# Performance work log

Measured on AMD Instinct MI355X. Metric: run time of the kernel, lower is better.

## Reference

```python
import jax, jax.numpy as jnp
import numpy as np

DT = 0.01
THETA = 1.0 / (2.0 - 2.0 ** (1.0 / 3.0))
C1 = THETA / 2.0
C2 = (1.0 - THETA) / 2.0
C3 = (1.0 - THETA) / 2.0
C4 = THETA / 2.0
D1 = THETA
D2 = 1.0 - 2.0 * THETA
D3 = THETA

B, DIM, RANK = 4096, 1024, 256


def setup_inputs() -> dict:
    key = jax.random.key(0)
    k0, k1, k2, k3, k4 = jax.random.split(key, 5)
    x = jax.random.normal(k0, (B, DIM), jnp.float32)
    v = jax.random.normal(k1, (B, DIM), jnp.float32)
    force = jax.random.normal(k2, (B, DIM), jnp.float32)
    # small-scale low-rank Christoffel factors for numerical stability over steps
    U = jax.random.normal(k3, (DIM, RANK), jnp.float32) * 0.02
    W = jax.random.normal(k4, (RANK, DIM), jnp.float32) * 0.02
    return {"x": x, "v": v, "force": force, "U": U, "W": W, "steps": 4}


def reference(x, v, force, U, W, steps):
    dt = DT  # dt_scale = 1.0

    def christoffel(tv, tx):
        # low-rank quadratic form in velocity: Gamma(v)_k = sum_r W[r,k] * ((v @ U)_r)^2
        h = tv @ U              # [B, RANK]
        return (h * h) @ W      # [B, DIM]

    def acceleration(tx, tv):
        return -christoffel(tv, tx) + force

    curr_x, curr_v = x, v
    for _ in range(steps):  # steps is a small static Python int
        x1 = curr_x + C1 * dt * curr_v
        v1 = curr_v + D1 * dt * acceleration(x1, curr_v)
        x2 = x1 + C2 * dt * v1
        v2 = v1 + D2 * dt * acceleration(x2, v1)
        x3 = x2 + C3 * dt * v2
        v3 = v2 + D3 * dt * acceleration(x3, v2)
        curr_x = x3 + C4 * dt * v3
        curr_v = v3
    return (curr_x, curr_v)
```

## Files before the change

kernel.cpp:

```cpp
#include <hip/hip_runtime.h>

typedef unsigned short ushort_t;
typedef float f32x4 __attribute__((ext_vector_type(4)));
typedef short s16x8 __attribute__((ext_vector_type(8)));

#define BROWS 4096
#define DIMK  1024
#define RANKK 256
#define TROWS 16
#define GPAD  (RANKK + 8)

#define DTF 0.01f
#define THETAF 1.35120719195965763f
#define C1F    0.675603595979828816f
#define C2F   (-0.175603595979828816f)
#define D1F    1.35120719195965763f
#define D2F   (-1.70241438391931526f)

__device__ __forceinline__ ushort_t f2bf(float f) {
    unsigned u = __builtin_bit_cast(unsigned, f);
    return (ushort_t)((u + 0x7FFFu + ((u >> 16) & 1u)) >> 16);
}

__global__ void fr_transpose_cast(const float* __restrict__ in,
                                  ushort_t* __restrict__ out, int R, int C) {
    __shared__ float tile[32][33];
    int tiles_c = C >> 5;
    int tr = blockIdx.x / tiles_c;
    int tc = blockIdx.x % tiles_c;
    int tx = threadIdx.x & 31;
    int ty = threadIdx.x >> 5;
#pragma unroll
    for (int i = 0; i < 32; i += 8)
        tile[ty + i][tx] = in[(size_t)(tr * 32 + ty + i) * C + tc * 32 + tx];
    __syncthreads();
#pragma unroll
    for (int i = 0; i < 32; i += 8)
        out[(size_t)(tc * 32 + ty + i) * R + tr * 32 + tx] = f2bf(tile[tx][ty + i]);
}

__global__ __launch_bounds__(512, 2) void fr_kernel(
    const float* __restrict__ x_in, const float* __restrict__ v_in,
    const float* __restrict__ f_in, const ushort_t* __restrict__ Ut,
    const ushort_t* __restrict__ Wt, const int* __restrict__ steps_p,
    float* __restrict__ out) {
    __shared__ ushort_t vb[TROWS * DIMK];
    __shared__ ushort_t gb[TROWS * GPAD];

    const int tid  = threadIdx.x;
    const int lane = tid & 63;
    const int wave = tid >> 6;
    const int m16  = lane & 15;
    const int g4   = lane >> 4;
    const int row0 = blockIdx.x * TROWS;
    const int n_acc = 3 * steps_p[0];

    float vreg[32], xreg[32], freg[32];
#pragma unroll
    for (int nt = 0; nt < 8; ++nt) {
#pragma unroll
        for (int r = 0; r < 4; ++r) {
            const int m = g4 * 4 + r;
            const int n = wave * 128 + nt * 16 + m16;
            const size_t gi = (size_t)(row0 + m) * DIMK + n;
            const float v0 = v_in[gi];
            vreg[nt * 4 + r] = v0;
            xreg[nt * 4 + r] = x_in[gi] + (C1F * DTF) * v0;
            freg[nt * 4 + r] = f_in[gi];
            vb[m * DIMK + (n ^ ((m & 7) << 3))] = f2bf(v0);
        }
    }
    __syncthreads();

    const s16x8* b0p = (const s16x8*)(Ut + (size_t)(wave * 32 + m16) * DIMK + g4 * 8);
    const s16x8* b1p = b0p + (16 * DIMK) / 8;
    const s16x8* bwp = (const s16x8*)(Wt + (size_t)(wave * 128 + m16) * RANKK + g4 * 8);
    const int n1a = wave * 32 + m16;
    const int n1b = n1a + 16;

    for (int j = 0; j < n_acc; ++j) {
        f32x4 h0 = {0.f, 0.f, 0.f, 0.f}, h1 = {0.f, 0.f, 0.f, 0.f};
#pragma unroll 8
        for (int kk = 0; kk < DIMK / 32; ++kk) {
            const int k0 = kk * 32 + g4 * 8;
            const s16x8 a = *(const s16x8*)&vb[m16 * DIMK + (k0 ^ ((m16 & 7) << 3))];
            const s16x8 b0 = b0p[kk * 4];
            const s16x8 b1 = b1p[kk * 4];
            h0 = __builtin_amdgcn_mfma_f32_16x16x32_bf16(a, b0, h0, 0, 0, 0);
            h1 = __builtin_amdgcn_mfma_f32_16x16x32_bf16(a, b1, h1, 0, 0, 0);
        }
#pragma unroll
        for (int r = 0; r < 4; ++r) {
            const int m = g4 * 4 + r;
            gb[m * GPAD + n1a] = f2bf(h0[r] * h0[r]);
            gb[m * GPAD + n1b] = f2bf(h1[r] * h1[r]);
        }
        __syncthreads();

        f32x4 acc[8];
#pragma unroll
        for (int nt = 0; nt < 8; ++nt) acc[nt] = (f32x4){0.f, 0.f, 0.f, 0.f};
#pragma unroll 2
        for (int kk = 0; kk < RANKK / 32; ++kk) {
            const int k0 = kk * 32 + g4 * 8;
            const s16x8 a = *(const s16x8*)&gb[m16 * GPAD + k0];
#pragma unroll
            for (int nt = 0; nt < 8; ++nt) {
                const s16x8 b = bwp[nt * 512 + kk * 4];
                acc[nt] = __builtin_amdgcn_mfma_f32_16x16x32_bf16(a, b, acc[nt], 0, 0, 0);
            }
        }

        const int ph = j - (j / 3) * 3;
        const float ddt = ((ph == 0) ? D1F : (ph == 1) ? D2F : D1F) * DTF;
        const float cdt = ((ph == 2) ? ((j == n_acc - 1) ? C1F : THETAF) : C2F) * DTF;
#pragma unroll
        for (int nt = 0; nt < 8; ++nt) {
#pragma unroll
            for (int r = 0; r < 4; ++r) {
                const int i = nt * 4 + r;
                const int m = g4 * 4 + r;
                const int n = wave * 128 + nt * 16 + m16;
                const float vn = vreg[i] + ddt * (freg[i] - acc[nt][r]);
                vreg[i] = vn;
                xreg[i] += cdt * vn;
                vb[m * DIMK + (n ^ ((m & 7) << 3))] = f2bf(vn);
            }
        }
        __syncthreads();
    }

    float* xo = out;
    float* vo = out + (size_t)BROWS * DIMK;
#pragma unroll
    for (int nt = 0; nt < 8; ++nt) {
#pragma unroll
        for (int r = 0; r < 4; ++r) {
            const int i = nt * 4 + r;
            const int m = g4 * 4 + r;
            const int n = wave * 128 + nt * 16 + m16;
            const size_t gi = (size_t)(row0 + m) * DIMK + n;
            xo[gi] = xreg[i];
            vo[gi] = vreg[i];
        }
    }
}

extern "C" void kernel_launch(void* const* d_in, const int* in_sizes, int n_in,
                              void* d_out, int out_size, void* d_ws, size_t ws_size,
                              hipStream_t stream) {
    const float* x = (const float*)d_in[0];
    const float* v = (const float*)d_in[1];
    const float* f = (const float*)d_in[2];
    const float* U = (const float*)d_in[3];
    const float* W = (const float*)d_in[4];
    const int* steps = (const int*)d_in[5];

    ushort_t* Ut = (ushort_t*)d_ws;
    ushort_t* Wt = Ut + (size_t)RANKK * DIMK;
    float* out = (float*)d_out;

    fr_transpose_cast<<<(DIMK / 32) * (RANKK / 32), 256, 0, stream>>>(U, Ut, DIMK, RANKK);
    fr_transpose_cast<<<(RANKK / 32) * (DIMK / 32), 256, 0, stream>>>(W, Wt, RANKK, DIMK);
    fr_kernel<<<BROWS / TROWS, 512, 0, stream>>>(x, v, f, Ut, Wt, steps, out);
}
```

Baseline: 369.3 us.

## Use 1024-thread blocks with software-pipelined weight prefetch and LDS-staged state

Doubles the block to 16 waves, so each wave owns 64 output columns and 16 rank columns. U and W are pre-packed into an MFMA-fragment-contiguous bf16 layout, and their fragments are prefetched in a rotating four-buffer register pipeline that runs across the two GEMM phases and iterations. x and force move out of registers into LDS (force packed as bf16) to cut register pressure. MFMAs are issued through inline asm with AGPR accumulators, and barriers become a raw lgkmcnt wait plus s_barrier. The cost is an LDS footprint of about 130KB, which limits occupancy to one block per CU, and the force term now loses precision from bf16 rounding.

```diff
diff --git a/kernel.cpp b/kernel.cpp
--- a/kernel.cpp
+++ b/kernel.cpp
@@ -1,6 +1,7 @@
 #include <hip/hip_runtime.h>
 
 typedef unsigned short ushort_t;
+typedef unsigned int u32;
 typedef float f32x4 __attribute__((ext_vector_type(4)));
 typedef short s16x8 __attribute__((ext_vector_type(8)));
 
@@ -8,7 +9,6 @@
 #define DIMK  1024
 #define RANKK 256
 #define TROWS 16
-#define GPAD  (RANKK + 8)
 
 #define DTF 0.01f
 #define THETAF 1.35120719195965763f
@@ -21,126 +21,182 @@
     unsigned u = __builtin_bit_cast(unsigned, f);
     return (ushort_t)((u + 0x7FFFu + ((u >> 16) & 1u)) >> 16);
 }
-
-__global__ void fr_transpose_cast(const float* __restrict__ in,
-                                  ushort_t* __restrict__ out, int R, int C) {
-    __shared__ float tile[32][33];
-    int tiles_c = C >> 5;
-    int tr = blockIdx.x / tiles_c;
-    int tc = blockIdx.x % tiles_c;
-    int tx = threadIdx.x & 31;
-    int ty = threadIdx.x >> 5;
-#pragma unroll
-    for (int i = 0; i < 32; i += 8)
-        tile[ty + i][tx] = in[(size_t)(tr * 32 + ty + i) * C + tc * 32 + tx];
-    __syncthreads();
-#pragma unroll
-    for (int i = 0; i < 32; i += 8)
-        out[(size_t)(tc * 32 + ty + i) * R + tr * 32 + tx] = f2bf(tile[tx][ty + i]);
-}
-
-__global__ __launch_bounds__(512, 2) void fr_kernel(
+__device__ __forceinline__ u32 pack2bf(float lo, float hi) {
+    return (u32)f2bf(lo) | ((u32)f2bf(hi) << 16);
+}
+__device__ __forceinline__ float unpk_lo(u32 u) {
+    return __builtin_bit_cast(float, u << 16);
+}
+__device__ __forceinline__ float unpk_hi(u32 u) {
+    return __builtin_bit_cast(float, u & 0xFFFF0000u);
+}
+
+__device__ __forceinline__ f32x4 mfma_agpr(s16x8 a, s16x8 b, f32x4 c) {
+    asm("v_mfma_f32_16x16x32_bf16 %0, %1, %2, %0" : "+a"(c) : "v"(a), "v"(b));
+    return c;
+}
+
+#define BAR() asm volatile("s_waitcnt lgkmcnt(0)\n\ts_barrier" ::: "memory")
+
+__global__ void fr_pack_u(const float* __restrict__ U, ushort_t* __restrict__ Ut2) {
+    const int o = blockIdx.x * 256 + threadIdx.x;
+    const int e = o & 7, g4 = (o >> 3) & 3, kk = (o >> 5) & 31;
+    const int m16 = (o >> 10) & 15, w = (o >> 14) & 15;
+    const int n = w * 16 + m16, k = kk * 32 + g4 * 8 + e;
+    Ut2[o] = f2bf(U[k * RANKK + n]);
+}
+__global__ void fr_pack_w(const float* __restrict__ W, ushort_t* __restrict__ Wt2) {
+    const int o = blockIdx.x * 256 + threadIdx.x;
+    const int e = o & 7, g4 = (o >> 3) & 3, nt = (o >> 5) & 3;
+    const int s = (o >> 7) & 7, m16 = (o >> 10) & 15, w = (o >> 14) & 15;
+    const int n = w * 64 + nt * 16 + m16, k = s * 32 + g4 * 8 + e;
+    Wt2[o] = f2bf(W[k * DIMK + n]);
+}
+
+
+#define L1(t, BUF) do {                                                       \
+    BUF[0] = *(const s16x8*)(up + (2 * (t)) * 32);                            \
+    BUF[1] = *(const s16x8*)(up + (2 * (t) + 1) * 32);                        \
+} while (0)
+
+#define G1(t, BUF) do {                                                       \
+    { const s16x8 a_ = *(const s16x8*)&vb[m16 * DIMK + (((2*(t))*32 + g4*8) ^ swz)];   \
+      h0 = mfma_agpr(a_, BUF[0], h0); }                                       \
+    { const s16x8 a_ = *(const s16x8*)&vb[m16 * DIMK + (((2*(t)+1)*32 + g4*8) ^ swz)]; \
+      h0 = mfma_agpr(a_, BUF[1], h0); }                                       \
+} while (0)
+
+#define L2(u, BUF) do {                                                       \
+    BUF[0] = *(const s16x8*)(wp + ((u) >> 1) * 128 + (((u) & 1) * 2) * 32);   \
+    BUF[1] = *(const s16x8*)(wp + ((u) >> 1) * 128 + (((u) & 1) * 2 + 1) * 32);\
+} while (0)
+
+#define G2(u, A2, BUF) do {                                                   \
+    acc[((u) & 1) * 2]     = mfma_agpr(A2, BUF[0], acc[((u) & 1) * 2]);       \
+    acc[((u) & 1) * 2 + 1] = mfma_agpr(A2, BUF[1], acc[((u) & 1) * 2 + 1]);   \
+} while (0)
+
+#define ARD(s) (*(const s16x8*)&gb[m16 * RANKK + (((s) * 32 + g4 * 8) ^ swz)])
+
+__global__ __launch_bounds__(1024) void fr_kernel(
     const float* __restrict__ x_in, const float* __restrict__ v_in,
-    const float* __restrict__ f_in, const ushort_t* __restrict__ Ut,
-    const ushort_t* __restrict__ Wt, const int* __restrict__ steps_p,
+    const float* __restrict__ f_in, const ushort_t* __restrict__ Ut2,
+    const ushort_t* __restrict__ Wt2, const int* __restrict__ steps_p,
     float* __restrict__ out) {
     __shared__ ushort_t vb[TROWS * DIMK];
-    __shared__ ushort_t gb[TROWS * GPAD];
+    __shared__ ushort_t gb[TROWS * RANKK];
+    __shared__ float    xs[TROWS * DIMK];
+    __shared__ u32      fb[8 * 1024];
 
     const int tid  = threadIdx.x;
     const int lane = tid & 63;
     const int wave = tid >> 6;
     const int m16  = lane & 15;
     const int g4   = lane >> 4;
+    const int swz  = (m16 & 7) << 3;
     const int row0 = blockIdx.x * TROWS;
     const int n_acc = 3 * steps_p[0];
 
-    float vreg[32], xreg[32], freg[32];
-#pragma unroll
-    for (int nt = 0; nt < 8; ++nt) {
+    float vreg[16], xdelta[16];
+#pragma unroll
+    for (int nt = 0; nt < 4; ++nt) {
+        float fv[4];
 #pragma unroll
         for (int r = 0; r < 4; ++r) {
             const int m = g4 * 4 + r;
-            const int n = wave * 128 + nt * 16 + m16;
+            const int n = wave * 64 + nt * 16 + m16;
             const size_t gi = (size_t)(row0 + m) * DIMK + n;
             const float v0 = v_in[gi];
-            vreg[nt * 4 + r] = v0;
-            xreg[nt * 4 + r] = x_in[gi] + (C1F * DTF) * v0;
-            freg[nt * 4 + r] = f_in[gi];
+            vreg[nt * 4 + r]   = v0;
+            xdelta[nt * 4 + r] = (C1F * DTF) * v0;
+            xs[m * DIMK + n]   = x_in[gi];
+            fv[r] = f_in[gi];
             vb[m * DIMK + (n ^ ((m & 7) << 3))] = f2bf(v0);
         }
+        fb[(nt * 2 + 0) * 1024 + tid] = pack2bf(fv[0], fv[1]);
+        fb[(nt * 2 + 1) * 1024 + tid] = pack2bf(fv[2], fv[3]);
     }
+
+    const ushort_t* up = Ut2 + (wave * 16 + m16) * 1024 + g4 * 8;
+    const ushort_t* wp = Wt2 + (wave * 16 + m16) * 1024 + g4 * 8;
+
+    s16x8 bA[2], bB[2], bC[2], bD[2];
+    L1(0, bA); L1(1, bB); L1(2, bC); L1(3, bD);
     __syncthreads();
 
-    const s16x8* b0p = (const s16x8*)(Ut + (size_t)(wave * 32 + m16) * DIMK + g4 * 8);
-    const s16x8* b1p = b0p + (16 * DIMK) / 8;
-    const s16x8* bwp = (const s16x8*)(Wt + (size_t)(wave * 128 + m16) * RANKK + g4 * 8);
-    const int n1a = wave * 32 + m16;
-    const int n1b = n1a + 16;
-
+    f32x4 acc[4];
     for (int j = 0; j < n_acc; ++j) {
-        f32x4 h0 = {0.f, 0.f, 0.f, 0.f}, h1 = {0.f, 0.f, 0.f, 0.f};
-#pragma unroll 8
-        for (int kk = 0; kk < DIMK / 32; ++kk) {
-            const int k0 = kk * 32 + g4 * 8;
-            const s16x8 a = *(const s16x8*)&vb[m16 * DIMK + (k0 ^ ((m16 & 7) << 3))];
-            const s16x8 b0 = b0p[kk * 4];
-            const s16x8 b1 = b1p[kk * 4];
-            h0 = __builtin_amdgcn_mfma_f32_16x16x32_bf16(a, b0, h0, 0, 0, 0);
-            h1 = __builtin_amdgcn_mfma_f32_16x16x32_bf16(a, b1, h1, 0, 0, 0);
-        }
-#pragma unroll
-        for (int r = 0; r < 4; ++r) {
-            const int m = g4 * 4 + r;
-            gb[m * GPAD + n1a] = f2bf(h0[r] * h0[r]);
-            gb[m * GPAD + n1b] = f2bf(h1[r] * h1[r]);
-        }
-        __syncthreads();
-
-        f32x4 acc[8];
-#pragma unroll
-        for (int nt = 0; nt < 8; ++nt) acc[nt] = (f32x4){0.f, 0.f, 0.f, 0.f};
-#pragma unroll 2
-        for (int kk = 0; kk < RANKK / 32; ++kk) {
-            const int k0 = kk * 32 + g4 * 8;
-            const s16x8 a = *(const s16x8*)&gb[m16 * GPAD + k0];
-#pragma unroll
-            for (int nt = 0; nt < 8; ++nt) {
-                const s16x8 b = bwp[nt * 512 + kk * 4];
-                acc[nt] = __builtin_amdgcn_mfma_f32_16x16x32_bf16(a, b, acc[nt], 0, 0, 0);
+        f32x4 h0 = {0.f, 0.f, 0.f, 0.f};
+        G1(0, bA);  L1(4, bA);
+        G1(1, bB);  L1(5, bB);
+        G1(2, bC);  L1(6, bC);
+        G1(3, bD);  L1(7, bD);
+        G1(4, bA);  L1(8, bA);
+        G1(5, bB);  L1(9, bB);
+        G1(6, bC);  L1(10, bC);
+        G1(7, bD);  L1(11, bD);
+        G1(8, bA);  L1(12, bA);
+        G1(9, bB);  L1(13, bB);
+        G1(10, bC); L1(14, bC);
+        G1(11, bD); L1(15, bD);
+        G1(12, bA); L2(0, bA);
+        G1(13, bB); L2(1, bB);
+        G1(14, bC); L2(2, bC);
+        G1(15, bD); L2(3, bD);
+
+        {
+            const int n1 = wave * 16 + m16;
+#pragma unroll
+            for (int r = 0; r < 4; ++r) {
+                const int m = g4 * 4 + r;
+                gb[m * RANKK + (n1 ^ ((m & 7) << 3))] = f2bf(h0[r] * h0[r]);
             }
         }
+        BAR();
+
+#pragma unroll
+        for (int q = 0; q < 4; ++q) acc[q] = (f32x4){0.f, 0.f, 0.f, 0.f};
+        { const s16x8 a0 = ARD(0); G2(0, a0, bA); L2(4, bA);  G2(1, a0, bB); L2(5, bB); }
+        { const s16x8 a1 = ARD(1); G2(2, a1, bC); L2(6, bC);  G2(3, a1, bD); L2(7, bD); }
+        { const s16x8 a2 = ARD(2); G2(4, a2, bA); L2(8, bA);  G2(5, a2, bB); L2(9, bB); }
+        { const s16x8 a3 = ARD(3); G2(6, a3, bC); L2(10, bC); G2(7, a3, bD); L2(11, bD); }
+        { const s16x8 a4 = ARD(4); G2(8, a4, bA); L2(12, bA); G2(9, a4, bB); L2(13, bB); }
+        { const s16x8 a5 = ARD(5); G2(10, a5, bC); L2(14, bC); G2(11, a5, bD); L2(15, bD); }
+        { const s16x8 a6 = ARD(6); G2(12, a6, bA); L1(0, bA);  G2(13, a6, bB); L1(1, bB); }
+        { const s16x8 a7 = ARD(7); G2(14, a7, bC); L1(2, bC);  G2(15, a7, bD); L1(3, bD); }
 
         const int ph = j - (j / 3) * 3;
-        const float ddt = ((ph == 0) ? D1F : (ph == 1) ? D2F : D1F) * DTF;
+        const float ddt = ((ph == 1) ? D2F : D1F) * DTF;
         const float cdt = ((ph == 2) ? ((j == n_acc - 1) ? C1F : THETAF) : C2F) * DTF;
 #pragma unroll
-        for (int nt = 0; nt < 8; ++nt) {
+        for (int nt = 0; nt < 4; ++nt) {
 #pragma unroll
             for (int r = 0; r < 4; ++r) {
                 const int i = nt * 4 + r;
                 const int m = g4 * 4 + r;
-                const int n = wave * 128 + nt * 16 + m16;
-                const float vn = vreg[i] + ddt * (freg[i] - acc[nt][r]);
+                const int n = wave * 64 + nt * 16 + m16;
+                const u32 pk = fb[(nt * 2 + (r >> 1)) * 1024 + tid];
+                const float fi = (r & 1) ? unpk_hi(pk) : unpk_lo(pk);
+                const float vn = vreg[i] + ddt * (fi - acc[nt][r]);
                 vreg[i] = vn;
-                xreg[i] += cdt * vn;
+                xdelta[i] += cdt * vn;
                 vb[m * DIMK + (n ^ ((m & 7) << 3))] = f2bf(vn);
             }
         }
-        __syncthreads();
+        BAR();
     }
 
     float* xo = out;
     float* vo = out + (size_t)BROWS * DIMK;
 #pragma unroll
-    for (int nt = 0; nt < 8; ++nt) {
+    for (int nt = 0; nt < 4; ++nt) {
 #pragma unroll
         for (int r = 0; r < 4; ++r) {
             const int i = nt * 4 + r;
             const int m = g4 * 4 + r;
-            const int n = wave * 128 + nt * 16 + m16;
+            const int n = wave * 64 + nt * 16 + m16;
             const size_t gi = (size_t)(row0 + m) * DIMK + n;
-            xo[gi] = xreg[i];
+            xo[gi] = xs[m * DIMK + n] + xdelta[i];
             vo[gi] = vreg[i];
         }
     }
@@ -156,11 +212,11 @@
     const float* W = (const float*)d_in[4];
     const int* steps = (const int*)d_in[5];
 
-    ushort_t* Ut = (ushort_t*)d_ws;
-    ushort_t* Wt = Ut + (size_t)RANKK * DIMK;
+    ushort_t* Ut2 = (ushort_t*)d_ws;
+    ushort_t* Wt2 = Ut2 + (size_t)RANKK * DIMK;
     float* out = (float*)d_out;
 
-    fr_transpose_cast<<<(DIMK / 32) * (RANKK / 32), 256, 0, stream>>>(U, Ut, DIMK, RANKK);
-    fr_transpose_cast<<<(RANKK / 32) * (DIMK / 32), 256, 0, stream>>>(W, Wt, RANKK, DIMK);
-    fr_kernel<<<BROWS / TROWS, 512, 0, stream>>>(x, v, f, Ut, Wt, steps, out);
-}
+    fr_pack_u<<<1024, 256, 0, stream>>>(U, Ut2);
+    fr_pack_w<<<1024, 256, 0, stream>>>(W, Wt2);
+    fr_kernel<<<BROWS / TROWS, 1024, 0, stream>>>(x, v, f, Ut2, Wt2, steps, out);
+}
```

Result: slower. 425.3 us (+15.2%).
